# Kernel optimization log

Hardware: AMD Instinct MI355X
Metric: run time of the kernel (lower is better)

## Reference

```python
import jax, jax.numpy as jnp
import numpy as np

RNN = 64      # rnn_hidden_dim
HID = 64      # hidden_dim
ENC = 3       # encoder_dim
NAG = 8       # n_agents
NACT = 14     # n_actions
CLIP = 0.2    # args.exp_clip (variance floor)
BN_EPS = 1e-5


def _bn(x, g, b):
    # BatchNorm1d in training mode: batch stats, biased variance
    m = x.mean(0)
    v = jnp.mean((x - m) ** 2, 0)
    return g * (x - m) * jax.lax.rsqrt(v + BN_EPS) + b


def setup_inputs() -> dict:
    key = jax.random.key(0)
    ks = jax.random.split(key, 16)
    B, INP = 8192, 96

    def w(k, shape, fan):
        return (jax.random.normal(k, shape, jnp.float32) / np.float32(np.sqrt(fan)))

    d = {}
    d["inputs"] = jax.random.normal(ks[0], (B * NAG, INP), jnp.float32)
    d["hidden_state"] = jax.random.normal(ks[1], (B * NAG, RNN), jnp.float32)
    d["noise"] = jax.random.normal(ks[2], (B, NAG, NAG * ENC), jnp.float32)
    d["fc1_w"] = w(ks[3], (INP, RNN), INP); d["fc1_b"] = jnp.zeros((RNN,), jnp.float32)
    d["w_ih"] = w(ks[4], (RNN, 3 * RNN), RNN); d["w_hh"] = w(ks[5], (RNN, 3 * RNN), RNN)
    d["b_ih"] = jnp.zeros((3 * RNN,), jnp.float32); d["b_hh"] = jnp.zeros((3 * RNN,), jnp.float32)
    d["aw1_w"] = w(ks[6], (RNN, HID), RNN); d["aw1_b"] = jnp.zeros((HID,), jnp.float32)
    d["aw_g"] = jnp.ones((HID,), jnp.float32); d["aw_be"] = jnp.zeros((HID,), jnp.float32)
    d["aw2_w"] = w(ks[7], (HID, 2 * NAG * ENC), HID); d["aw2_b"] = jnp.zeros((2 * NAG * ENC,), jnp.float32)
    d["po1_w"] = w(ks[8], (2 * RNN, HID), 2 * RNN); d["po1_b"] = jnp.zeros((HID,), jnp.float32)
    d["po_g"] = jnp.ones((HID,), jnp.float32); d["po_be"] = jnp.zeros((HID,), jnp.float32)
    d["po2_w"] = w(ks[9], (HID, 2 * ENC), HID); d["po2_b"] = jnp.zeros((2 * ENC,), jnp.float32)
    d["fc2_w"] = w(ks[10], (RNN + ENC * NAG, NACT), RNN + ENC * NAG); d["fc2_b"] = jnp.zeros((NACT,), jnp.float32)
    return d


def reference(inputs, hidden_state, noise,
              fc1_w, fc1_b, w_ih, w_hh, b_ih, b_hh,
              aw1_w, aw1_b, aw_g, aw_be, aw2_w, aw2_b,
              po1_w, po1_b, po_g, po_be, po2_w, po2_b,
              fc2_w, fc2_b):
    B, n, enc = noise.shape[0], NAG, ENC

    x = jax.nn.relu(inputs @ fc1_w + fc1_b)                      # [B*n, RNN]
    h_in = hidden_state.reshape(-1, RNN)

    # torch GRUCell
    gi = x @ w_ih + b_ih
    gh = h_in @ w_hh + b_hh
    ir, iz, i_n = jnp.split(gi, 3, axis=-1)
    hr, hz, h_n = jnp.split(gh, 3, axis=-1)
    r = jax.nn.sigmoid(ir + hr)
    z = jax.nn.sigmoid(iz + hz)
    nt = jnp.tanh(i_n + r * h_n)
    h = (1.0 - z) * nt + z * h_in                                # [B*n, RNN]

    # awareness encoder
    a = jax.nn.relu(_bn(h @ aw1_w + aw1_b, aw_g, aw_be))
    aw = (a @ aw2_w + aw2_b).reshape(B, n, 2 * n * enc)
    mu = aw[:, :, : n * enc]
    sigma = jnp.maximum(jnp.exp(aw[:, :, n * enc:]), CLIP)       # variance
    c = (mu + jnp.sqrt(sigma) * noise).reshape(-1, n * enc)      # rsample

    x_out = jnp.concatenate([h, c], axis=-1) @ fc2_w + fc2_b     # [B*n, NACT]

    # poster branch (training mode): all-pairs concat H[b, j, id] = [h[b,id], h[b,j]]
    hd = jax.lax.stop_gradient(h).reshape(B, n, RNN)
    Hi = jnp.broadcast_to(hd[:, None, :, :], (B, n, n, RNN))     # axis2 = id
    Hj = jnp.broadcast_to(hd[:, :, None, :], (B, n, n, RNN))     # axis1 = j
    H = jnp.concatenate([Hi, Hj], axis=-1).reshape(-1, 2 * RNN)  # [B*n*n, 2*RNN]

    p = jax.nn.relu(_bn(H @ po1_w + po1_b, po_g, po_be))
    out = (p @ po2_w + po2_b).reshape(B, n, 2 * n * enc)
    mu1 = out[:, :, : n * enc]
    sigma1 = jnp.maximum(jnp.exp(out[:, :, n * enc:]), CLIP)

    # KL between diagonal Gaussians (sigma, sigma1 are variances)
    kl = 0.5 * (jnp.log(sigma1 / sigma) + (sigma + (mu - mu1) ** 2) / sigma1 - 1.0)
    KL = kl.mean(axis=-1).mean(axis=-1, keepdims=True)           # [B, 1]
    return (x_out, h, KL)
```

## Files before the change

kernel.cpp:

```cpp
#include <hip/hip_runtime.h>
#include <math.h>

#define NROWS 65536
#define NB    8192
#define STAT_OFF  0
#define WPACK_OFF 448
#define OUT_XOUT 0
#define OUT_H    917504
#define OUT_KL   5111808

typedef __attribute__((ext_vector_type(8))) short bhalf8;
typedef __attribute__((ext_vector_type(4))) float floatx4;
typedef __attribute__((ext_vector_type(4))) unsigned short u16x4;

__device__ __forceinline__ float sigmf(float x) { return 1.0f / (1.0f + __expf(-x)); }
__device__ __forceinline__ float tanhfast(float x) {
    x = fminf(fmaxf(x, -15.f), 15.f);
    float e = __expf(-2.f * x);
    return (1.f - e) / (1.f + e);
}
__device__ __forceinline__ unsigned short f2bf(float f) {
    unsigned int u = __float_as_uint(f);
    u += 0x7FFFu + ((u >> 16) & 1u);
    return (unsigned short)(u >> 16);
}

__global__ void k_prep(const float* __restrict__ fc1_w,
                       const float* __restrict__ w_ih, const float* __restrict__ w_hh,
                       const float* __restrict__ aw1_w, const float* __restrict__ po1_w,
                       const float* __restrict__ aw2_w, const float* __restrict__ fc2_w,
                       float* __restrict__ ws)
{
    const int t = threadIdx.x;
    if (blockIdx.x == 0)
        for (int i = t; i < 448; i += 256) ws[STAT_OFF + i] = 0.f;

    unsigned short* wpk = (unsigned short*)(ws + WPACK_OFF);
    for (int f = blockIdx.x * 256 + t; f < 5952; f += gridDim.x * 256) {
        int lane, c, tile;
        const float* src;
        int colbase, krowstride, kofs = 0, kmax = 1 << 30, colmax = 16;
        if (f < 768) {
            tile = f / 192; c = (f % 192) / 64; lane = f % 64;
            src = fc1_w; krowstride = 64; colbase = tile * 16;
        } else if (f < 3840) {
            int f2 = f - 768;
            tile = f2 / 128; c = (f2 % 128) / 64; lane = f2 % 64;
            if (tile < 12) { src = w_ih; colbase = tile * 16; }
            else           { src = w_hh; colbase = (tile - 12) * 16; }
            krowstride = 192;
        } else if (f < 5376) {
            int f3 = f - 3840;
            tile = f3 / 128; c = (f3 % 128) / 64; lane = f3 % 64;
            if (tile < 4)       { src = aw1_w; colbase = tile * 16; }
            else if (tile < 8)  { src = po1_w; colbase = (tile - 4) * 16; }
            else                { src = po1_w; colbase = (tile - 8) * 16; kofs = 64; }
            krowstride = 64;
        } else if (f < 5760) {
            int f4 = f - 5376;
            tile = f4 / 128; c = (f4 % 128) / 64; lane = f4 % 64;
            src = aw2_w; krowstride = 48; colbase = tile * 16;
        } else {
            int f5 = f - 5760;
            c = f5 / 64; lane = f5 % 64;
            src = fc2_w; krowstride = 14; colbase = 0;
            kmax = 88; colmax = 14;
        }
        int n = lane & 15, quad = lane >> 4;
        int col = colbase + n;
        unsigned short o[8];
        #pragma unroll
        for (int j = 0; j < 8; j++) {
            int k = c * 32 + quad * 8 + j + kofs;
            float v = (k < kmax && n < colmax) ? src[(size_t)k * krowstride + col] : 0.f;
            o[j] = f2bf(v);
        }
        u16x4 lo, hi;
        lo.x = o[0]; lo.y = o[1]; lo.z = o[2]; lo.w = o[3];
        hi.x = o[4]; hi.y = o[5]; hi.z = o[6]; hi.w = o[7];
        *(u16x4*)&wpk[f * 8]     = lo;
        *(u16x4*)&wpk[f * 8 + 4] = hi;
    }
}

__global__ __launch_bounds__(256, 2) void k_front(
    const float* __restrict__ inp, const float* __restrict__ hin,
    const float* __restrict__ fc1_b,
    const float* __restrict__ b_ih, const float* __restrict__ b_hh,
    const float* __restrict__ aw1_b,
    float* __restrict__ h_out, float* __restrict__ ws)
{
    __shared__ __align__(16) unsigned short s_inpb[128 * 104];
    __shared__ __align__(16) unsigned short s_hinb[128 * 88];
    __shared__ __align__(16) unsigned short s_xb[128 * 88];
    __shared__ float s_stat[448];

    const int t = threadIdx.x;
    const int row0 = blockIdx.x * 128;
    const int lane = t & 63;
    const int w = t >> 6;
    const int n16 = lane & 15;
    const int quad = lane >> 4;

    {
        const float* gi = inp + (size_t)row0 * 96;
        for (int i = t; i < 3072; i += 256) {
            int r = i / 24, c4 = (i - r * 24) * 4;
            float4 v = *(const float4*)&gi[r * 96 + c4];
            u16x4 p; p.x = f2bf(v.x); p.y = f2bf(v.y); p.z = f2bf(v.z); p.w = f2bf(v.w);
            *(u16x4*)&s_inpb[r * 104 + c4] = p;
        }
        const float* gh = hin + (size_t)row0 * 64;
        for (int i = t; i < 2048; i += 256) {
            int r = i >> 4, c4 = (i & 15) * 4;
            float4 v = *(const float4*)&gh[r * 64 + c4];
            u16x4 p; p.x = f2bf(v.x); p.y = f2bf(v.y); p.z = f2bf(v.z); p.w = f2bf(v.w);
            *(u16x4*)&s_hinb[r * 88 + c4] = p;
        }
    }
    for (int i = t; i < 448; i += 256) s_stat[i] = 0.f;
    __syncthreads();

    const bhalf8* wp1 = (const bhalf8*)((const unsigned short*)(ws + WPACK_OFF));
    const bhalf8* wp2 = wp1 + 768;
    const bhalf8* wp3 = wp1 + 3840;

    {
        bhalf8 ai[2][3];
        #pragma unroll
        for (int u = 0; u < 2; u++) {
            int mr = w * 32 + u * 16 + n16;
            ai[u][0] = *(const bhalf8*)&s_inpb[mr * 104 + 0  + quad * 8];
            ai[u][1] = *(const bhalf8*)&s_inpb[mr * 104 + 32 + quad * 8];
            ai[u][2] = *(const bhalf8*)&s_inpb[mr * 104 + 64 + quad * 8];
        }
        #pragma unroll
        for (int g = 0; g < 4; g++) {
            bhalf8 f0 = wp1[(g * 3 + 0) * 64 + lane];
            bhalf8 f1 = wp1[(g * 3 + 1) * 64 + lane];
            bhalf8 f2 = wp1[(g * 3 + 2) * 64 + lane];
            int col = g * 16 + n16;
            float bb = fc1_b[col];
            #pragma unroll
            for (int u = 0; u < 2; u++) {
                floatx4 d = {0.f, 0.f, 0.f, 0.f};
                d = __builtin_amdgcn_mfma_f32_16x16x32_bf16(ai[u][0], f0, d, 0, 0, 0);
                d = __builtin_amdgcn_mfma_f32_16x16x32_bf16(ai[u][1], f1, d, 0, 0, 0);
                d = __builtin_amdgcn_mfma_f32_16x16x32_bf16(ai[u][2], f2, d, 0, 0, 0);
                #pragma unroll
                for (int q = 0; q < 4; q++) {
                    float xv = fmaxf(d[q] + bb, 0.f);
                    s_xb[(w * 32 + u * 16 + quad * 4 + q) * 88 + col] = f2bf(xv);
                }
            }
        }
    }

    floatx4 gr[2][4], gz[2][4], gn[2][4], gh2[2][4];
    {
        bhalf8 ax0[2], ax1[2], ah0[2], ah1[2];
        #pragma unroll
        for (int u = 0; u < 2; u++) {
            int mr = w * 32 + u * 16 + n16;
            ax0[u] = *(const bhalf8*)&s_xb[mr * 88 + 0  + quad * 8];
            ax1[u] = *(const bhalf8*)&s_xb[mr * 88 + 32 + quad * 8];
            ah0[u] = *(const bhalf8*)&s_hinb[mr * 88 + 0  + quad * 8];
            ah1[u] = *(const bhalf8*)&s_hinb[mr * 88 + 32 + quad * 8];
        }
        #pragma unroll
        for (int g = 0; g < 4; g++) {
            {
                bhalf8 f0 = wp2[((0 + g) * 2 + 0) * 64 + lane];
                bhalf8 f1 = wp2[((0 + g) * 2 + 1) * 64 + lane];
                bhalf8 f2 = wp2[((12 + g) * 2 + 0) * 64 + lane];
                bhalf8 f3 = wp2[((12 + g) * 2 + 1) * 64 + lane];
                #pragma unroll
                for (int u = 0; u < 2; u++) {
                    floatx4 d = {0.f, 0.f, 0.f, 0.f};
                    d = __builtin_amdgcn_mfma_f32_16x16x32_bf16(ax0[u], f0, d, 0, 0, 0);
                    d = __builtin_amdgcn_mfma_f32_16x16x32_bf16(ax1[u], f1, d, 0, 0, 0);
                    d = __builtin_amdgcn_mfma_f32_16x16x32_bf16(ah0[u], f2, d, 0, 0, 0);
                    d = __builtin_amdgcn_mfma_f32_16x16x32_bf16(ah1[u], f3, d, 0, 0, 0);
                    gr[u][g] = d;
                }
            }
            {
                bhalf8 f0 = wp2[((4 + g) * 2 + 0) * 64 + lane];
                bhalf8 f1 = wp2[((4 + g) * 2 + 1) * 64 + lane];
                bhalf8 f2 = wp2[((16 + g) * 2 + 0) * 64 + lane];
                bhalf8 f3 = wp2[((16 + g) * 2 + 1) * 64 + lane];
                #pragma unroll
                for (int u = 0; u < 2; u++) {
                    floatx4 d = {0.f, 0.f, 0.f, 0.f};
                    d = __builtin_amdgcn_mfma_f32_16x16x32_bf16(ax0[u], f0, d, 0, 0, 0);
                    d = __builtin_amdgcn_mfma_f32_16x16x32_bf16(ax1[u], f1, d, 0, 0, 0);
                    d = __builtin_amdgcn_mfma_f32_16x16x32_bf16(ah0[u], f2, d, 0, 0, 0);
                    d = __builtin_amdgcn_mfma_f32_16x16x32_bf16(ah1[u], f3, d, 0, 0, 0);
                    gz[u][g] = d;
                }
            }
            {
                bhalf8 f0 = wp2[((8 + g) * 2 + 0) * 64 + lane];
                bhalf8 f1 = wp2[((8 + g) * 2 + 1) * 64 + lane];
                #pragma unroll
                for (int u = 0; u < 2; u++) {
                    floatx4 d = {0.f, 0.f, 0.f, 0.f};
                    d = __builtin_amdgcn_mfma_f32_16x16x32_bf16(ax0[u], f0, d, 0, 0, 0);
                    d = __builtin_amdgcn_mfma_f32_16x16x32_bf16(ax1[u], f1, d, 0, 0, 0);
                    gn[u][g] = d;
                }
            }
            {
                bhalf8 f0 = wp2[((20 + g) * 2 + 0) * 64 + lane];
                bhalf8 f1 = wp2[((20 + g) * 2 + 1) * 64 + lane];
                #pragma unroll
                for (int u = 0; u < 2; u++) {
                    floatx4 d = {0.f, 0.f, 0.f, 0.f};
                    d = __builtin_amdgcn_mfma_f32_16x16x32_bf16(ah0[u], f0, d, 0, 0, 0);
                    d = __builtin_amdgcn_mfma_f32_16x16x32_bf16(ah1[u], f1, d, 0, 0, 0);
                    gh2[u][g] = d;
                }
            }
        }
    }
    __syncthreads();

    unsigned short* s_hb = s_inpb;
    #pragma unroll
    for (int g = 0; g < 4; g++) {
        int col = g * 16 + n16;
        float br_ = b_ih[col] + b_hh[col];
        float bz_ = b_ih[64 + col] + b_hh[64 + col];
        float bin_ = b_ih[128 + col];
        float bhn_ = b_hh[128 + col];
        #pragma unroll
        for (int u = 0; u < 2; u++) {
            #pragma unroll
            for (int q = 0; q < 4; q++) {
                int lrow = w * 32 + u * 16 + quad * 4 + q;
                size_t grow = (size_t)(row0 + lrow);
                float r  = sigmf(gr[u][g][q] + br_);
                float z  = sigmf(gz[u][g][q] + bz_);
                float nt = tanhfast(gn[u][g][q] + bin_ + r * (gh2[u][g][q] + bhn_));
                float hp = hin[grow * 64 + col];
                float h  = (1.f - z) * nt + z * hp;
                h_out[grow * 64 + col] = h;
                s_hb[lrow * 88 + col] = f2bf(h);
            }
        }
    }

    {
        bhalf8 bh0[2], bh1[2];
        #pragma unroll
        for (int u = 0; u < 2; u++) {
            int mr = w * 32 + u * 16 + n16;
            bh0[u] = *(const bhalf8*)&s_hb[mr * 88 + 0  + quad * 8];
            bh1[u] = *(const bhalf8*)&s_hb[mr * 88 + 32 + quad * 8];
        }
        floatx4 g3[2][12];
        #pragma unroll
        for (int tt = 0; tt < 12; tt++) {
            bhalf8 f0 = wp3[(tt * 2 + 0) * 64 + lane];
            bhalf8 f1 = wp3[(tt * 2 + 1) * 64 + lane];
            #pragma unroll
            for (int u = 0; u < 2; u++) {
                floatx4 d = {0.f, 0.f, 0.f, 0.f};
                d = __builtin_amdgcn_mfma_f32_16x16x32_bf16(bh0[u], f0, d, 0, 0, 0);
                d = __builtin_amdgcn_mfma_f32_16x16x32_bf16(bh1[u], f1, d, 0, 0, 0);
                g3[u][tt] = d;
            }
        }
        #pragma unroll
        for (int g = 0; g < 4; g++) {
            int col = g * 16 + n16;
            float ab = aw1_b[col];
            float s1 = 0.f, s2 = 0.f, suq = 0.f, svq = 0.f;
            float su[2] = {0.f, 0.f}, sv[2] = {0.f, 0.f};
            #pragma unroll
            for (int u = 0; u < 2; u++) {
                #pragma unroll
                for (int q = 0; q < 4; q++) {
                    float a = g3[u][g][q] + ab; s1 += a; s2 += a * a;
                    float uv = g3[u][4 + g][q]; su[u] += uv; suq += uv * uv;
                    float vv = g3[u][8 + g][q]; sv[u] += vv; svq += vv * vv;
                }
            }
            #pragma unroll
            for (int u = 0; u < 2; u++) {
                float u8 = su[u] + __shfl_xor(su[u], 16, 64);
                float v8 = sv[u] + __shfl_xor(sv[u], 16, 64);
                if ((quad & 1) == 0)
                    atomicAdd(&s_stat[384 + col], u8 * v8 * (1.f / 64.f));
            }
            float sut = su[0] + su[1];
            float svt = sv[0] + sv[1];
            float t1 = s1 + __shfl_xor(s1, 16, 64);  t1 += __shfl_xor(t1, 32, 64);
            float t2 = s2 + __shfl_xor(s2, 16, 64);  t2 += __shfl_xor(t2, 32, 64);
            float t3 = sut + __shfl_xor(sut, 16, 64); t3 += __shfl_xor(t3, 32, 64);
            float t4 = suq + __shfl_xor(suq, 16, 64); t4 += __shfl_xor(t4, 32, 64);
            float t5 = svt + __shfl_xor(svt, 16, 64); t5 += __shfl_xor(t5, 32, 64);
            float t6 = svq + __shfl_xor(svq, 16, 64); t6 += __shfl_xor(t6, 32, 64);
            if (quad == 0) {
                atomicAdd(&s_stat[col], t1);
                atomicAdd(&s_stat[64 + col], t2);
                atomicAdd(&s_stat[128 + col], t3);
                atomicAdd(&s_stat[192 + col], t4);
                atomicAdd(&s_stat[256 + col], t5);
                atomicAdd(&s_stat[320 + col], t6);
            }
        }
    }
    __syncthreads();
    if (t < 64) {
        float* gs = ws + STAT_OFF;
        #pragma unroll
        for (int q = 0; q < 7; q++)
            atomicAdd(&gs[q * 64 + t], s_stat[q * 64 + t]);
    }
}

__global__ __launch_bounds__(128) void k_heads(
    const float* __restrict__ h_glob, const float* __restrict__ noise,
    const float* __restrict__ aw1_b, const float* __restrict__ aw2_b,
    const float* __restrict__ fc2_b, const float* __restrict__ po2_b,
    const float* __restrict__ aw_g, const float* __restrict__ aw_be,
    const float* __restrict__ po_g, const float* __restrict__ po_be,
    const float* __restrict__ po1_b, const float* __restrict__ po2_w,
    const float* __restrict__ ws, float* __restrict__ out)
{
    __shared__ __align__(16) unsigned short s_hb[32 * 104];
    __shared__ __align__(16) float s_Uf[32 * 68];
    __shared__ __align__(16) float s_Vf[32 * 68];
    __shared__ float s_ms[32 * 48];
    __shared__ __align__(16) float s_u2[32 * 48];
    __shared__ __align__(16) float s_dv[640];
    __shared__ float s_kl[32];

    const int t = threadIdx.x;
    const int row0 = blockIdx.x * 32;
    const int b0 = blockIdx.x * 4;
    const int lane = t & 63;
    const int w = t >> 6;
    const int n16 = lane & 15;
    const int quad = lane >> 4;
    const int mrow = w * 16 + n16;

    if (t < 64) {
        const float* st = ws + STAT_OFF;
        const float invN = 1.f / 65536.f;
        float am = st[t] * invN;
        float av = st[64 + t] * invN - am * am;
        float asc = aw_g[t] * rsqrtf(av + 1e-5f);
        s_dv[t] = asc;
        s_dv[64 + t] = aw_be[t] - asc * am;
        float Eu = st[128 + t] * invN;
        float vu = st[192 + t] * invN - Eu * Eu;
        float Ev = st[256 + t] * invN;
        float vv = st[320 + t] * invN - Ev * Ev;
        float cov = st[384 + t] * (1.f / 8192.f) - Eu * Ev;
        float my = Eu + Ev + po1_b[t];
        float vy = vu + vv + 2.f * cov;
        float psc = po_g[t] * rsqrtf(vy + 1e-5f);
        s_dv[128 + t] = psc;
        s_dv[192 + t] = po_be[t] + psc * (po1_b[t] - my);
    }
    for (int i = t; i < 384; i += 128) {
        int d = i >> 6, c = i & 63;
        s_dv[256 + i] = po2_w[c * 6 + d];
    }

    {
        const float* gh = h_glob + (size_t)row0 * 64;
        for (int i = t; i < 512; i += 128) {
            int r = i >> 4, c4 = (i & 15) * 4;
            float4 v = *(const float4*)&gh[r * 64 + c4];
            u16x4 p; p.x = f2bf(v.x); p.y = f2bf(v.y); p.z = f2bf(v.z); p.w = f2bf(v.w);
            *(u16x4*)&s_hb[r * 104 + c4] = p;
        }
        for (int i = t; i < 64; i += 128) {
            int r = i >> 1, c4 = 88 + (i & 1) * 4;
            u16x4 z; z.x = 0; z.y = 0; z.z = 0; z.w = 0;
            *(u16x4*)&s_hb[r * 104 + c4] = z;
        }
    }
    __syncthreads();

    const bhalf8* wp3  = ((const bhalf8*)((const unsigned short*)(ws + WPACK_OFF))) + 3840;
    const bhalf8* wpa2 = wp3 + 1536;
    const bhalf8* wpf2 = wpa2 + 384;
    unsigned short* s_ab = (unsigned short*)s_u2;

    {
        bhalf8 ah0 = *(const bhalf8*)&s_hb[mrow * 104 + 0  + quad * 8];
        bhalf8 ah1 = *(const bhalf8*)&s_hb[mrow * 104 + 32 + quad * 8];
        floatx4 g3[12];
        #pragma unroll
        for (int tt = 0; tt < 12; tt++) {
            floatx4 d = {0.f, 0.f, 0.f, 0.f};
            d = __builtin_amdgcn_mfma_f32_16x16x32_bf16(ah0, wp3[(tt * 2 + 0) * 64 + lane], d, 0, 0, 0);
            d = __builtin_amdgcn_mfma_f32_16x16x32_bf16(ah1, wp3[(tt * 2 + 1) * 64 + lane], d, 0, 0, 0);
            g3[tt] = d;
        }
        #pragma unroll
        for (int g = 0; g < 4; g++) {
            int col = g * 16 + n16;
            float ab = aw1_b[col];
            float asc = s_dv[col], ash = s_dv[64 + col];
            float psc = s_dv[128 + col], psh = s_dv[192 + col];
            #pragma unroll
            for (int q = 0; q < 4; q++) {
                int lrow = w * 16 + quad * 4 + q;
                float a = fmaxf(asc * (g3[g][q] + ab) + ash, 0.f);
                s_ab[lrow * 72 + col] = f2bf(a);
                s_Uf[lrow * 68 + col] = psc * g3[4 + g][q];
                s_Vf[lrow * 68 + col] = psc * g3[8 + g][q] + psh;
            }
        }
    }
    __syncthreads();

    {
        bhalf8 aa0 = *(const bhalf8*)&s_ab[mrow * 72 + 0  + quad * 8];
        bhalf8 aa1 = *(const bhalf8*)&s_ab[mrow * 72 + 32 + quad * 8];
        #pragma unroll
        for (int g = 0; g < 3; g++) {
            floatx4 d = {0.f, 0.f, 0.f, 0.f};
            d = __builtin_amdgcn_mfma_f32_16x16x32_bf16(aa0, wpa2[(g * 2 + 0) * 64 + lane], d, 0, 0, 0);
            d = __builtin_amdgcn_mfma_f32_16x16x32_bf16(aa1, wpa2[(g * 2 + 1) * 64 + lane], d, 0, 0, 0);
            int col = g * 16 + n16;
            float bb = aw2_b[col];
            #pragma unroll
            for (int q = 0; q < 4; q++) {
                int lrow = w * 16 + quad * 4 + q;
                float v = d[q] + bb;
                s_ms[lrow * 48 + col] = (col < 24) ? v : fmaxf(__expf(v), 0.2f);
            }
        }
    }
    __syncthreads();

    for (int i = t; i < 768; i += 128) {
        int r = i / 24, m = i - r * 24;
        float c = s_ms[r * 48 + m] + sqrtf(s_ms[r * 48 + 24 + m]) * noise[(size_t)(row0 + r) * 24 + m];
        s_hb[r * 104 + 64 + m] = f2bf(c);
    }
    __syncthreads();

    {
        bhalf8 hc0 = *(const bhalf8*)&s_hb[mrow * 104 + 0  + quad * 8];
        bhalf8 hc1 = *(const bhalf8*)&s_hb[mrow * 104 + 32 + quad * 8];
        bhalf8 hc2 = *(const bhalf8*)&s_hb[mrow * 104 + 64 + quad * 8];
        floatx4 d = {0.f, 0.f, 0.f, 0.f};
        d = __builtin_amdgcn_mfma_f32_16x16x32_bf16(hc0, wpf2[0 * 64 + lane], d, 0, 0, 0);
        d = __builtin_amdgcn_mfma_f32_16x16x32_bf16(hc1, wpf2[1 * 64 + lane], d, 0, 0, 0);
        d = __builtin_amdgcn_mfma_f32_16x16x32_bf16(hc2, wpf2[2 * 64 + lane], d, 0, 0, 0);
        if (n16 < 14) {
            float bb = fc2_b[n16];
            float* xout = out + OUT_XOUT;
            #pragma unroll
            for (int q = 0; q < 4; q++) {
                size_t grow = (size_t)(row0 + w * 16 + quad * 4 + q);
                xout[grow * 14 + n16] = d[q] + bb;
            }
        }
    }
    __syncthreads();

    float* s_out = s_u2;
    {
        const float* p2t = s_dv + 256;
        const int bl = t >> 5;
        const int rem = t & 31;
        const int i_ = rem >> 2;
        const int j0 = (rem & 3) * 2;
        float acc[2][6];
        #pragma unroll
        for (int jj = 0; jj < 2; jj++)
            #pragma unroll
            for (int d = 0; d < 6; d++) acc[jj][d] = 0.f;

        for (int c = 0; c < 64; c += 4) {
            float vv[4]; *(float4*)vv = *(const float4*)&s_Vf[(bl * 8 + i_) * 68 + c];
            float wv[6][4];
            #pragma unroll
            for (int d = 0; d < 6; d++) *(float4*)wv[d] = *(const float4*)&p2t[d * 64 + c];
            #pragma unroll
            for (int jj = 0; jj < 2; jj++) {
                float uu[4]; *(float4*)uu = *(const float4*)&s_Uf[(bl * 8 + j0 + jj) * 68 + c];
                float p[4];
                #pragma unroll
                for (int q = 0; q < 4; q++) p[q] = fmaxf(uu[q] + vv[q], 0.f);
                #pragma unroll
                for (int d = 0; d < 6; d++)
                    acc[jj][d] += p[0] * wv[d][0] + p[1] * wv[d][1] + p[2] * wv[d][2] + p[3] * wv[d][3];
            }
        }
        #pragma unroll
        for (int jj = 0; jj < 2; jj++)
            #pragma unroll
            for (int d = 0; d < 6; d++)
                s_out[(bl * 8 + i_) * 48 + (j0 + jj) * 6 + d] = acc[jj][d] + po2_b[d];
    }
    __syncthreads();

    if (t < 32) {
        float s = 0.f;
        #pragma unroll 4
        for (int m = 0; m < 24; m++) {
            float mu0 = s_ms[t * 48 + m];
            float sg0 = s_ms[t * 48 + 24 + m];
            float mu1 = s_out[t * 48 + m];
            float sg1 = fmaxf(__expf(s_out[t * 48 + 24 + m]), 0.2f);
            float d0 = mu0 - mu1;
            s += __logf(sg1 / sg0) + (sg0 + d0 * d0) / sg1 - 1.f;
        }
        s_kl[t] = s;
    }
    __syncthreads();
    if (t < 4) {
        float s = 0.f;
        #pragma unroll
        for (int i = 0; i < 8; i++) s += s_kl[t * 8 + i];
        out[OUT_KL + b0 + t] = s * (0.5f / 192.f);
    }
}

extern "C" void kernel_launch(void* const* d_in, const int* in_sizes, int n_in,
                              void* d_out, int out_size, void* d_ws, size_t ws_size,
                              hipStream_t stream)
{
    (void)in_sizes; (void)n_in; (void)out_size; (void)ws_size;
    const float* inp   = (const float*)d_in[0];
    const float* hin   = (const float*)d_in[1];
    const float* noise = (const float*)d_in[2];
    const float* fc1_w = (const float*)d_in[3];
    const float* fc1_b = (const float*)d_in[4];
    const float* w_ih  = (const float*)d_in[5];
    const float* w_hh  = (const float*)d_in[6];
    const float* b_ih  = (const float*)d_in[7];
    const float* b_hh  = (const float*)d_in[8];
    const float* aw1_w = (const float*)d_in[9];
    const float* aw1_b = (const float*)d_in[10];
    const float* aw_g  = (const float*)d_in[11];
    const float* aw_be = (const float*)d_in[12];
    const float* aw2_w = (const float*)d_in[13];
    const float* aw2_b = (const float*)d_in[14];
    const float* po1_w = (const float*)d_in[15];
    const float* po1_b = (const float*)d_in[16];
    const float* po_g  = (const float*)d_in[17];
    const float* po_be = (const float*)d_in[18];
    const float* po2_w = (const float*)d_in[19];
    const float* po2_b = (const float*)d_in[20];
    const float* fc2_w = (const float*)d_in[21];
    const float* fc2_b = (const float*)d_in[22];
    float* out = (float*)d_out;
    float* ws  = (float*)d_ws;

    hipLaunchKernelGGL(k_prep,  dim3(24),   dim3(256), 0, stream,
                       fc1_w, w_ih, w_hh, aw1_w, po1_w, aw2_w, fc2_w, ws);
    hipLaunchKernelGGL(k_front, dim3(512),  dim3(256), 0, stream,
                       inp, hin, fc1_b, b_ih, b_hh, aw1_b, out + OUT_H, ws);
    hipLaunchKernelGGL(k_heads, dim3(2048), dim3(128), 0, stream,
                       out + OUT_H, noise, aw1_b, aw2_b, fc2_b, po2_b,
                       aw_g, aw_be, po_g, po_be, po1_b, po2_w, ws, out);
}
```

Baseline: 197.7 us.

## Load front-kernel operands straight to registers, shrink LDS, store poster U/V as bf16

The front kernel no longer stages the input and hidden tiles in shared memory. Each lane loads its MFMA fragments directly from global memory and packs them to bf16 in registers. GRU and aw1/poster matmuls are now computed one 16-column group at a time instead of holding all gate accumulators live, and a single small LDS buffer is reused, which allows raising launch bounds to 4 blocks per SM. In the back kernel, the U/V poster projections are stored as bf16, one barrier is dropped and MFMAs are computed per group. This trades fewer uncoalesced global reads for less LDS and register pressure, and adds bf16 rounding on U/V.

Result: no change. 197.2 us (-0.2%).

```diff
diff --git a/kernel.cpp b/kernel.cpp
--- a/kernel.cpp
+++ b/kernel.cpp
@@ -23,6 +23,17 @@
     unsigned int u = __float_as_uint(f);
     u += 0x7FFFu + ((u >> 16) & 1u);
     return (unsigned short)(u >> 16);
+}
+__device__ __forceinline__ float bf2f(unsigned short s) {
+    return __uint_as_float(((unsigned int)s) << 16);
+}
+__device__ __forceinline__ bhalf8 pack8(float4 a, float4 b) {
+    bhalf8 r;
+    r[0] = (short)f2bf(a.x); r[1] = (short)f2bf(a.y);
+    r[2] = (short)f2bf(a.z); r[3] = (short)f2bf(a.w);
+    r[4] = (short)f2bf(b.x); r[5] = (short)f2bf(b.y);
+    r[6] = (short)f2bf(b.z); r[7] = (short)f2bf(b.w);
+    return r;
 }
 
 __global__ void k_prep(const float* __restrict__ fc1_w,
@@ -83,16 +94,14 @@
     }
 }
 
-__global__ __launch_bounds__(256, 2) void k_front(
+__global__ __launch_bounds__(256, 4) void k_front(
     const float* __restrict__ inp, const float* __restrict__ hin,
     const float* __restrict__ fc1_b,
     const float* __restrict__ b_ih, const float* __restrict__ b_hh,
     const float* __restrict__ aw1_b,
     float* __restrict__ h_out, float* __restrict__ ws)
 {
-    __shared__ __align__(16) unsigned short s_inpb[128 * 104];
-    __shared__ __align__(16) unsigned short s_hinb[128 * 88];
-    __shared__ __align__(16) unsigned short s_xb[128 * 88];
+    __shared__ __align__(16) unsigned short s_xb[128 * 80];
     __shared__ float s_stat[448];
 
     const int t = threadIdx.x;
@@ -102,22 +111,6 @@
     const int n16 = lane & 15;
     const int quad = lane >> 4;
 
-    {
-        const float* gi = inp + (size_t)row0 * 96;
-        for (int i = t; i < 3072; i += 256) {
-            int r = i / 24, c4 = (i - r * 24) * 4;
-            float4 v = *(const float4*)&gi[r * 96 + c4];
-            u16x4 p; p.x = f2bf(v.x); p.y = f2bf(v.y); p.z = f2bf(v.z); p.w = f2bf(v.w);
-            *(u16x4*)&s_inpb[r * 104 + c4] = p;
-        }
-        const float* gh = hin + (size_t)row0 * 64;
-        for (int i = t; i < 2048; i += 256) {
-            int r = i >> 4, c4 = (i & 15) * 4;
-            float4 v = *(const float4*)&gh[r * 64 + c4];
-            u16x4 p; p.x = f2bf(v.x); p.y = f2bf(v.y); p.z = f2bf(v.z); p.w = f2bf(v.w);
-            *(u16x4*)&s_hinb[r * 88 + c4] = p;
-        }
-    }
     for (int i = t; i < 448; i += 256) s_stat[i] = 0.f;
     __syncthreads();
 
@@ -125,110 +118,101 @@
     const bhalf8* wp2 = wp1 + 768;
     const bhalf8* wp3 = wp1 + 3840;
 
-    {
-        bhalf8 ai[2][3];
+    bhalf8 ai[2][3], ahf[2][2];
+    #pragma unroll
+    for (int u = 0; u < 2; u++) {
+        const float* gi = inp + (size_t)(row0 + w * 32 + u * 16 + n16) * 96 + quad * 8;
+        #pragma unroll
+        for (int kc = 0; kc < 3; kc++)
+            ai[u][kc] = pack8(*(const float4*)&gi[kc * 32], *(const float4*)&gi[kc * 32 + 4]);
+        const float* gh = hin + (size_t)(row0 + w * 32 + u * 16 + n16) * 64 + quad * 8;
+        #pragma unroll
+        for (int kc = 0; kc < 2; kc++)
+            ahf[u][kc] = pack8(*(const float4*)&gh[kc * 32], *(const float4*)&gh[kc * 32 + 4]);
+    }
+
+    #pragma unroll
+    for (int g = 0; g < 4; g++) {
+        bhalf8 f0 = wp1[(g * 3 + 0) * 64 + lane];
+        bhalf8 f1 = wp1[(g * 3 + 1) * 64 + lane];
+        bhalf8 f2 = wp1[(g * 3 + 2) * 64 + lane];
+        int col = g * 16 + n16;
+        float bb = fc1_b[col];
         #pragma unroll
         for (int u = 0; u < 2; u++) {
-            int mr = w * 32 + u * 16 + n16;
-            ai[u][0] = *(const bhalf8*)&s_inpb[mr * 104 + 0  + quad * 8];
-            ai[u][1] = *(const bhalf8*)&s_inpb[mr * 104 + 32 + quad * 8];
-            ai[u][2] = *(const bhalf8*)&s_inpb[mr * 104 + 64 + quad * 8];
-        }
-        #pragma unroll
-        for (int g = 0; g < 4; g++) {
-            bhalf8 f0 = wp1[(g * 3 + 0) * 64 + lane];
-            bhalf8 f1 = wp1[(g * 3 + 1) * 64 + lane];
-            bhalf8 f2 = wp1[(g * 3 + 2) * 64 + lane];
-            int col = g * 16 + n16;
-            float bb = fc1_b[col];
-            #pragma unroll
-            for (int u = 0; u < 2; u++) {
-                floatx4 d = {0.f, 0.f, 0.f, 0.f};
-                d = __builtin_amdgcn_mfma_f32_16x16x32_bf16(ai[u][0], f0, d, 0, 0, 0);
-                d = __builtin_amdgcn_mfma_f32_16x16x32_bf16(ai[u][1], f1, d, 0, 0, 0);
-                d = __builtin_amdgcn_mfma_f32_16x16x32_bf16(ai[u][2], f2, d, 0, 0, 0);
-                #pragma unroll
-                for (int q = 0; q < 4; q++) {
-                    float xv = fmaxf(d[q] + bb, 0.f);
-                    s_xb[(w * 32 + u * 16 + quad * 4 + q) * 88 + col] = f2bf(xv);
-                }
-            }
-        }
-    }
-
-    floatx4 gr[2][4], gz[2][4], gn[2][4], gh2[2][4];
-    {
-        bhalf8 ax0[2], ax1[2], ah0[2], ah1[2];
-        #pragma unroll
-        for (int u = 0; u < 2; u++) {
-            int mr = w * 32 + u * 16 + n16;
-            ax0[u] = *(const bhalf8*)&s_xb[mr * 88 + 0  + quad * 8];
-            ax1[u] = *(const bhalf8*)&s_xb[mr * 88 + 32 + quad * 8];
-            ah0[u] = *(const bhalf8*)&s_hinb[mr * 88 + 0  + quad * 8];
-            ah1[u] = *(const bhalf8*)&s_hinb[mr * 88 + 32 + quad * 8];
-        }
-        #pragma unroll
-        for (int g = 0; g < 4; g++) {
-            {
-                bhalf8 f0 = wp2[((0 + g) * 2 + 0) * 64 + lane];
-                bhalf8 f1 = wp2[((0 + g) * 2 + 1) * 64 + lane];
-                bhalf8 f2 = wp2[((12 + g) * 2 + 0) * 64 + lane];
-                bhalf8 f3 = wp2[((12 + g) * 2 + 1) * 64 + lane];
-                #pragma unroll
-                for (int u = 0; u < 2; u++) {
-                    floatx4 d = {0.f, 0.f, 0.f, 0.f};
-                    d = __builtin_amdgcn_mfma_f32_16x16x32_bf16(ax0[u], f0, d, 0, 0, 0);
-                    d = __builtin_amdgcn_mfma_f32_16x16x32_bf16(ax1[u], f1, d, 0, 0, 0);
-                    d = __builtin_amdgcn_mfma_f32_16x16x32_bf16(ah0[u], f2, d, 0, 0, 0);
-                    d = __builtin_amdgcn_mfma_f32_16x16x32_bf16(ah1[u], f3, d, 0, 0, 0);
-                    gr[u][g] = d;
-                }
-            }
-            {
-                bhalf8 f0 = wp2[((4 + g) * 2 + 0) * 64 + lane];
-                bhalf8 f1 = wp2[((4 + g) * 2 + 1) * 64 + lane];
-                bhalf8 f2 = wp2[((16 + g) * 2 + 0) * 64 + lane];
-                bhalf8 f3 = wp2[((16 + g) * 2 + 1) * 64 + lane];
-                #pragma unroll
-                for (int u = 0; u < 2; u++) {
-                    floatx4 d = {0.f, 0.f, 0.f, 0.f};
-                    d = __builtin_amdgcn_mfma_f32_16x16x32_bf16(ax0[u], f0, d, 0, 0, 0);
-                    d = __builtin_amdgcn_mfma_f32_16x16x32_bf16(ax1[u], f1, d, 0, 0, 0);
-                    d = __builtin_amdgcn_mfma_f32_16x16x32_bf16(ah0[u], f2, d, 0, 0, 0);
-                    d = __builtin_amdgcn_mfma_f32_16x16x32_bf16(ah1[u], f3, d, 0, 0, 0);
-                    gz[u][g] = d;
-                }
-            }
-            {
-                bhalf8 f0 = wp2[((8 + g) * 2 + 0) * 64 + lane];
-                bhalf8 f1 = wp2[((8 + g) * 2 + 1) * 64 + lane];
-                #pragma unroll
-                for (int u = 0; u < 2; u++) {
-                    floatx4 d = {0.f, 0.f, 0.f, 0.f};
-                    d = __builtin_amdgcn_mfma_f32_16x16x32_bf16(ax0[u], f0, d, 0, 0, 0);
-                    d = __builtin_amdgcn_mfma_f32_16x16x32_bf16(ax1[u], f1, d, 0, 0, 0);
-                    gn[u][g] = d;
-                }
-            }
-            {
-                bhalf8 f0 = wp2[((20 + g) * 2 + 0) * 64 + lane];
-                bhalf8 f1 = wp2[((20 + g) * 2 + 1) * 64 + lane];
-                #pragma unroll
-                for (int u = 0; u < 2; u++) {
-                    floatx4 d = {0.f, 0.f, 0.f, 0.f};
-                    d = __builtin_amdgcn_mfma_f32_16x16x32_bf16(ah0[u], f0, d, 0, 0, 0);
-                    d = __builtin_amdgcn_mfma_f32_16x16x32_bf16(ah1[u], f1, d, 0, 0, 0);
-                    gh2[u][g] = d;
-                }
-            }
-        }
-    }
-    __syncthreads();
-
-    unsigned short* s_hb = s_inpb;
+            floatx4 d = {0.f, 0.f, 0.f, 0.f};
+            d = __builtin_amdgcn_mfma_f32_16x16x32_bf16(ai[u][0], f0, d, 0, 0, 0);
+            d = __builtin_amdgcn_mfma_f32_16x16x32_bf16(ai[u][1], f1, d, 0, 0, 0);
+            d = __builtin_amdgcn_mfma_f32_16x16x32_bf16(ai[u][2], f2, d, 0, 0, 0);
+            #pragma unroll
+            for (int q = 0; q < 4; q++)
+                s_xb[(w * 32 + u * 16 + quad * 4 + q) * 80 + col] = f2bf(fmaxf(d[q] + bb, 0.f));
+        }
+    }
+    bhalf8 ax[2][2];
+    #pragma unroll
+    for (int u = 0; u < 2; u++) {
+        int mr = w * 32 + u * 16 + n16;
+        ax[u][0] = *(const bhalf8*)&s_xb[mr * 80 + 0  + quad * 8];
+        ax[u][1] = *(const bhalf8*)&s_xb[mr * 80 + 32 + quad * 8];
+    }
+
     #pragma unroll
     for (int g = 0; g < 4; g++) {
         int col = g * 16 + n16;
+        floatx4 dr[2], dz[2], dn[2], dh[2];
+        {
+            bhalf8 f0 = wp2[((0 + g) * 2 + 0) * 64 + lane];
+            bhalf8 f1 = wp2[((0 + g) * 2 + 1) * 64 + lane];
+            bhalf8 f2 = wp2[((12 + g) * 2 + 0) * 64 + lane];
+            bhalf8 f3 = wp2[((12 + g) * 2 + 1) * 64 + lane];
+            #pragma unroll
+            for (int u = 0; u < 2; u++) {
+                floatx4 d = {0.f, 0.f, 0.f, 0.f};
+                d = __builtin_amdgcn_mfma_f32_16x16x32_bf16(ax[u][0], f0, d, 0, 0, 0);
+                d = __builtin_amdgcn_mfma_f32_16x16x32_bf16(ax[u][1], f1, d, 0, 0, 0);
+                d = __builtin_amdgcn_mfma_f32_16x16x32_bf16(ahf[u][0], f2, d, 0, 0, 0);
+                d = __builtin_amdgcn_mfma_f32_16x16x32_bf16(ahf[u][1], f3, d, 0, 0, 0);
+                dr[u] = d;
+            }
+        }
+        {
+            bhalf8 f0 = wp2[((4 + g) * 2 + 0) * 64 + lane];
+            bhalf8 f1 = wp2[((4 + g) * 2 + 1) * 64 + lane];
+            bhalf8 f2 = wp2[((16 + g) * 2 + 0) * 64 + lane];
+            bhalf8 f3 = wp2[((16 + g) * 2 + 1) * 64 + lane];
+            #pragma unroll
+            for (int u = 0; u < 2; u++) {
+                floatx4 d = {0.f, 0.f, 0.f, 0.f};
+                d = __builtin_amdgcn_mfma_f32_16x16x32_bf16(ax[u][0], f0, d, 0, 0, 0);
+                d = __builtin_amdgcn_mfma_f32_16x16x32_bf16(ax[u][1], f1, d, 0, 0, 0);
+                d = __builtin_amdgcn_mfma_f32_16x16x32_bf16(ahf[u][0], f2, d, 0, 0, 0);
+                d = __builtin_amdgcn_mfma_f32_16x16x32_bf16(ahf[u][1], f3, d, 0, 0, 0);
+                dz[u] = d;
+            }
+        }
+        {
+            bhalf8 f0 = wp2[((8 + g) * 2 + 0) * 64 + lane];
+            bhalf8 f1 = wp2[((8 + g) * 2 + 1) * 64 + lane];
+            #pragma unroll
+            for (int u = 0; u < 2; u++) {
+                floatx4 d = {0.f, 0.f, 0.f, 0.f};
+                d = __builtin_amdgcn_mfma_f32_16x16x32_bf16(ax[u][0], f0, d, 0, 0, 0);
+                d = __builtin_amdgcn_mfma_f32_16x16x32_bf16(ax[u][1], f1, d, 0, 0, 0);
+                dn[u] = d;
+            }
+        }
+        {
+            bhalf8 f0 = wp2[((20 + g) * 2 + 0) * 64 + lane];
+            bhalf8 f1 = wp2[((20 + g) * 2 + 1) * 64 + lane];
+            #pragma unroll
+            for (int u = 0; u < 2; u++) {
+                floatx4 d = {0.f, 0.f, 0.f, 0.f};
+                d = __builtin_amdgcn_mfma_f32_16x16x32_bf16(ahf[u][0], f0, d, 0, 0, 0);
+                d = __builtin_amdgcn_mfma_f32_16x16x32_bf16(ahf[u][1], f1, d, 0, 0, 0);
+                dh[u] = d;
+            }
+        }
         float br_ = b_ih[col] + b_hh[col];
         float bz_ = b_ih[64 + col] + b_hh[64 + col];
         float bin_ = b_ih[128 + col];
@@ -239,76 +223,96 @@
             for (int q = 0; q < 4; q++) {
                 int lrow = w * 32 + u * 16 + quad * 4 + q;
                 size_t grow = (size_t)(row0 + lrow);
-                float r  = sigmf(gr[u][g][q] + br_);
-                float z  = sigmf(gz[u][g][q] + bz_);
-                float nt = tanhfast(gn[u][g][q] + bin_ + r * (gh2[u][g][q] + bhn_));
+                float r  = sigmf(dr[u][q] + br_);
+                float z  = sigmf(dz[u][q] + bz_);
+                float nt = tanhfast(dn[u][q] + bin_ + r * (dh[u][q] + bhn_));
                 float hp = hin[grow * 64 + col];
                 float h  = (1.f - z) * nt + z * hp;
                 h_out[grow * 64 + col] = h;
-                s_hb[lrow * 88 + col] = f2bf(h);
-            }
-        }
-    }
-
-    {
-        bhalf8 bh0[2], bh1[2];
+                s_xb[lrow * 80 + col] = f2bf(h);
+            }
+        }
+    }
+
+    bhalf8 hh[2][2];
+    #pragma unroll
+    for (int u = 0; u < 2; u++) {
+        int mr = w * 32 + u * 16 + n16;
+        hh[u][0] = *(const bhalf8*)&s_xb[mr * 80 + 0  + quad * 8];
+        hh[u][1] = *(const bhalf8*)&s_xb[mr * 80 + 32 + quad * 8];
+    }
+
+    #pragma unroll
+    for (int g = 0; g < 4; g++) {
+        int col = g * 16 + n16;
+        floatx4 da[2], du[2], dvv[2];
+        {
+            bhalf8 f0 = wp3[(g * 2 + 0) * 64 + lane];
+            bhalf8 f1 = wp3[(g * 2 + 1) * 64 + lane];
+            #pragma unroll
+            for (int u = 0; u < 2; u++) {
+                floatx4 d = {0.f, 0.f, 0.f, 0.f};
+                d = __builtin_amdgcn_mfma_f32_16x16x32_bf16(hh[u][0], f0, d, 0, 0, 0);
+                d = __builtin_amdgcn_mfma_f32_16x16x32_bf16(hh[u][1], f1, d, 0, 0, 0);
+                da[u] = d;
+            }
+        }
+        {
+            bhalf8 f0 = wp3[((4 + g) * 2 + 0) * 64 + lane];
+            bhalf8 f1 = wp3[((4 + g) * 2 + 1) * 64 + lane];
+            #pragma unroll
+            for (int u = 0; u < 2; u++) {
+                floatx4 d = {0.f, 0.f, 0.f, 0.f};
+                d = __builtin_amdgcn_mfma_f32_16x16x32_bf16(hh[u][0], f0, d, 0, 0, 0);
+                d = __builtin_amdgcn_mfma_f32_16x16x32_bf16(hh[u][1], f1, d, 0, 0, 0);
+                du[u] = d;
+            }
+        }
+        {
+            bhalf8 f0 = wp3[((8 + g) * 2 + 0) * 64 + lane];
+            bhalf8 f1 = wp3[((8 + g) * 2 + 1) * 64 + lane];
+            #pragma unroll
+            for (int u = 0; u < 2; u++) {
+                floatx4 d = {0.f, 0.f, 0.f, 0.f};
+                d = __builtin_amdgcn_mfma_f32_16x16x32_bf16(hh[u][0], f0, d, 0, 0, 0);
+                d = __builtin_amdgcn_mfma_f32_16x16x32_bf16(hh[u][1], f1, d, 0, 0, 0);
+                dvv[u] = d;
+            }
+        }
+        float ab = aw1_b[col];
+        float s1 = 0.f, s2 = 0.f, suq = 0.f, svq = 0.f;
+        float su[2] = {0.f, 0.f}, sv[2] = {0.f, 0.f};
         #pragma unroll
         for (int u = 0; u < 2; u++) {
-            int mr = w * 32 + u * 16 + n16;
-            bh0[u] = *(const bhalf8*)&s_hb[mr * 88 + 0  + quad * 8];
-            bh1[u] = *(const bhalf8*)&s_hb[mr * 88 + 32 + quad * 8];
-        }
-        floatx4 g3[2][12];
-        #pragma unroll
-        for (int tt = 0; tt < 12; tt++) {
-            bhalf8 f0 = wp3[(tt * 2 + 0) * 64 + lane];
-            bhalf8 f1 = wp3[(tt * 2 + 1) * 64 + lane];
-            #pragma unroll
-            for (int u = 0; u < 2; u++) {
-                floatx4 d = {0.f, 0.f, 0.f, 0.f};
-                d = __builtin_amdgcn_mfma_f32_16x16x32_bf16(bh0[u], f0, d, 0, 0, 0);
-                d = __builtin_amdgcn_mfma_f32_16x16x32_bf16(bh1[u], f1, d, 0, 0, 0);
-                g3[u][tt] = d;
-            }
-        }
-        #pragma unroll
-        for (int g = 0; g < 4; g++) {
-            int col = g * 16 + n16;
-            float ab = aw1_b[col];
-            float s1 = 0.f, s2 = 0.f, suq = 0.f, svq = 0.f;
-            float su[2] = {0.f, 0.f}, sv[2] = {0.f, 0.f};
-            #pragma unroll
-            for (int u = 0; u < 2; u++) {
-                #pragma unroll
-                for (int q = 0; q < 4; q++) {
-                    float a = g3[u][g][q] + ab; s1 += a; s2 += a * a;
-                    float uv = g3[u][4 + g][q]; su[u] += uv; suq += uv * uv;
-                    float vv = g3[u][8 + g][q]; sv[u] += vv; svq += vv * vv;
-                }
-            }
-            #pragma unroll
-            for (int u = 0; u < 2; u++) {
-                float u8 = su[u] + __shfl_xor(su[u], 16, 64);
-                float v8 = sv[u] + __shfl_xor(sv[u], 16, 64);
-                if ((quad & 1) == 0)
-                    atomicAdd(&s_stat[384 + col], u8 * v8 * (1.f / 64.f));
-            }
-            float sut = su[0] + su[1];
-            float svt = sv[0] + sv[1];
-            float t1 = s1 + __shfl_xor(s1, 16, 64);  t1 += __shfl_xor(t1, 32, 64);
-            float t2 = s2 + __shfl_xor(s2, 16, 64);  t2 += __shfl_xor(t2, 32, 64);
-            float t3 = sut + __shfl_xor(sut, 16, 64); t3 += __shfl_xor(t3, 32, 64);
-            float t4 = suq + __shfl_xor(suq, 16, 64); t4 += __shfl_xor(t4, 32, 64);
-            float t5 = svt + __shfl_xor(svt, 16, 64); t5 += __shfl_xor(t5, 32, 64);
-            float t6 = svq + __shfl_xor(svq, 16, 64); t6 += __shfl_xor(t6, 32, 64);
-            if (quad == 0) {
-                atomicAdd(&s_stat[col], t1);
-                atomicAdd(&s_stat[64 + col], t2);
-                atomicAdd(&s_stat[128 + col], t3);
-                atomicAdd(&s_stat[192 + col], t4);
-                atomicAdd(&s_stat[256 + col], t5);
-                atomicAdd(&s_stat[320 + col], t6);
-            }
+            #pragma unroll
+            for (int q = 0; q < 4; q++) {
+                float a = da[u][q] + ab; s1 += a; s2 += a * a;
+                float uv = du[u][q]; su[u] += uv; suq += uv * uv;
+                float vv = dvv[u][q]; sv[u] += vv; svq += vv * vv;
+            }
+        }
+        #pragma unroll
+        for (int u = 0; u < 2; u++) {
+            float u8 = su[u] + __shfl_xor(su[u], 16, 64);
+            float v8 = sv[u] + __shfl_xor(sv[u], 16, 64);
+            if ((quad & 1) == 0)
+                atomicAdd(&s_stat[384 + col], u8 * v8 * (1.f / 64.f));
+        }
+        float sut = su[0] + su[1];
+        float svt = sv[0] + sv[1];
+        float t1 = s1 + __shfl_xor(s1, 16, 64);   t1 += __shfl_xor(t1, 32, 64);
+        float t2 = s2 + __shfl_xor(s2, 16, 64);   t2 += __shfl_xor(t2, 32, 64);
+        float t3 = sut + __shfl_xor(sut, 16, 64); t3 += __shfl_xor(t3, 32, 64);
+        float t4 = suq + __shfl_xor(suq, 16, 64); t4 += __shfl_xor(t4, 32, 64);
+        float t5 = svt + __shfl_xor(svt, 16, 64); t5 += __shfl_xor(t5, 32, 64);
+        float t6 = svq + __shfl_xor(svq, 16, 64); t6 += __shfl_xor(t6, 32, 64);
+        if (quad == 0) {
+            atomicAdd(&s_stat[col], t1);
+            atomicAdd(&s_stat[64 + col], t2);
+            atomicAdd(&s_stat[128 + col], t3);
+            atomicAdd(&s_stat[192 + col], t4);
+            atomicAdd(&s_stat[256 + col], t5);
+            atomicAdd(&s_stat[320 + col], t6);
         }
     }
     __syncthreads();
@@ -330,10 +334,10 @@
     const float* __restrict__ ws, float* __restrict__ out)
 {
     __shared__ __align__(16) unsigned short s_hb[32 * 104];
-    __shared__ __align__(16) float s_Uf[32 * 68];
-    __shared__ __align__(16) float s_Vf[32 * 68];
+    __shared__ __align__(16) unsigned short s_Ub[32 * 80];
+    __shared__ __align__(16) unsigned short s_Vb[32 * 80];
     __shared__ float s_ms[32 * 48];
-    __shared__ __align__(16) float s_u2[32 * 48];
+    __shared__ __align__(16) float s_out[32 * 48];
     __shared__ __align__(16) float s_dv[640];
     __shared__ float s_kl[32];
 
@@ -389,40 +393,37 @@
     const bhalf8* wp3  = ((const bhalf8*)((const unsigned short*)(ws + WPACK_OFF))) + 3840;
     const bhalf8* wpa2 = wp3 + 1536;
     const bhalf8* wpf2 = wpa2 + 384;
-    unsigned short* s_ab = (unsigned short*)s_u2;
+    unsigned short* s_ab = (unsigned short*)s_out;
 
     {
         bhalf8 ah0 = *(const bhalf8*)&s_hb[mrow * 104 + 0  + quad * 8];
         bhalf8 ah1 = *(const bhalf8*)&s_hb[mrow * 104 + 32 + quad * 8];
-        floatx4 g3[12];
-        #pragma unroll
-        for (int tt = 0; tt < 12; tt++) {
-            floatx4 d = {0.f, 0.f, 0.f, 0.f};
-            d = __builtin_amdgcn_mfma_f32_16x16x32_bf16(ah0, wp3[(tt * 2 + 0) * 64 + lane], d, 0, 0, 0);
-            d = __builtin_amdgcn_mfma_f32_16x16x32_bf16(ah1, wp3[(tt * 2 + 1) * 64 + lane], d, 0, 0, 0);
-            g3[tt] = d;
-        }
         #pragma unroll
         for (int g = 0; g < 4; g++) {
             int col = g * 16 + n16;
+            floatx4 da = {0.f, 0.f, 0.f, 0.f}, duu = {0.f, 0.f, 0.f, 0.f}, dvv = {0.f, 0.f, 0.f, 0.f};
+            da  = __builtin_amdgcn_mfma_f32_16x16x32_bf16(ah0, wp3[(g * 2 + 0) * 64 + lane], da, 0, 0, 0);
+            da  = __builtin_amdgcn_mfma_f32_16x16x32_bf16(ah1, wp3[(g * 2 + 1) * 64 + lane], da, 0, 0, 0);
+            duu = __builtin_amdgcn_mfma_f32_16x16x32_bf16(ah0, wp3[((4 + g) * 2 + 0) * 64 + lane], duu, 0, 0, 0);
+            duu = __builtin_amdgcn_mfma_f32_16x16x32_bf16(ah1, wp3[((4 + g) * 2 + 1) * 64 + lane], duu, 0, 0, 0);
+            dvv = __builtin_amdgcn_mfma_f32_16x16x32_bf16(ah0, wp3[((8 + g) * 2 + 0) * 64 + lane], dvv, 0, 0, 0);
+            dvv = __builtin_amdgcn_mfma_f32_16x16x32_bf16(ah1, wp3[((8 + g) * 2 + 1) * 64 + lane], dvv, 0, 0, 0);
             float ab = aw1_b[col];
             float asc = s_dv[col], ash = s_dv[64 + col];
             float psc = s_dv[128 + col], psh = s_dv[192 + col];
             #pragma unroll
             for (int q = 0; q < 4; q++) {
                 int lrow = w * 16 + quad * 4 + q;
-                float a = fmaxf(asc * (g3[g][q] + ab) + ash, 0.f);
-                s_ab[lrow * 72 + col] = f2bf(a);
-                s_Uf[lrow * 68 + col] = psc * g3[4 + g][q];
-                s_Vf[lrow * 68 + col] = psc * g3[8 + g][q] + psh;
-            }
-        }
-    }
-    __syncthreads();
+                s_ab[lrow * 80 + col] = f2bf(fmaxf(asc * (da[q] + ab) + ash, 0.f));
+                s_Ub[lrow * 80 + col] = f2bf(psc * duu[q]);
+                s_Vb[lrow * 80 + col] = f2bf(psc * dvv[q] + psh);
+            }
+        }
+    }
 
     {
-        bhalf8 aa0 = *(const bhalf8*)&s_ab[mrow * 72 + 0  + quad * 8];
-        bhalf8 aa1 = *(const bhalf8*)&s_ab[mrow * 72 + 32 + quad * 8];
+        bhalf8 aa0 = *(const bhalf8*)&s_ab[mrow * 80 + 0  + quad * 8];
+        bhalf8 aa1 = *(const bhalf8*)&s_ab[mrow * 80 + 32 + quad * 8];
         #pragma unroll
         for (int g = 0; g < 3; g++) {
             floatx4 d = {0.f, 0.f, 0.f, 0.f};
@@ -467,7 +468,6 @@
     }
     __syncthreads();
 
-    float* s_out = s_u2;
     {
         const float* p2t = s_dv + 256;
         const int bl = t >> 5;
@@ -481,16 +481,19 @@
             for (int d = 0; d < 6; d++) acc[jj][d] = 0.f;
 
         for (int c = 0; c < 64; c += 4) {
-            float vv[4]; *(float4*)vv = *(const float4*)&s_Vf[(bl * 8 + i_) * 68 + c];
+            u16x4 vb4 = *(const u16x4*)&s_Vb[(bl * 8 + i_) * 80 + c];
+            float vv[4] = {bf2f(vb4.x), bf2f(vb4.y), bf2f(vb4.z), bf2f(vb4.w)};
             float wv[6][4];
             #pragma unroll
             for (int d = 0; d < 6; d++) *(float4*)wv[d] = *(const float4*)&p2t[d * 64 + c];
             #pragma unroll
             for (int jj = 0; jj < 2; jj++) {
-                float uu[4]; *(float4*)uu = *(const float4*)&s_Uf[(bl * 8 + j0 + jj) * 68 + c];
+                u16x4 ub4 = *(const u16x4*)&s_Ub[(bl * 8 + j0 + jj) * 80 + c];
                 float p[4];
-                #pragma unroll
-                for (int q = 0; q < 4; q++) p[q] = fmaxf(uu[q] + vv[q], 0.f);
+                p[0] = fmaxf(bf2f(ub4.x) + vv[0], 0.f);
+                p[1] = fmaxf(bf2f(ub4.y) + vv[1], 0.f);
+                p[2] = fmaxf(bf2f(ub4.z) + vv[2], 0.f);
+                p[3] = fmaxf(bf2f(ub4.w) + vv[3], 0.f);
                 #pragma unroll
                 for (int d = 0; d < 6; d++)
                     acc[jj][d] += p[0] * wv[d][0] + p[1] * wv[d][1] + p[2] * wv[d][2] + p[3] * wv[d][3];
```
